# Kernel tuning notes

Hardware: AMD Instinct MI355X
Metric: run time of the kernel (lower is better)

## Reference

```python
import jax, jax.numpy as jnp
import numpy as np

N = 100000      # nodes
E = 640000      # edges
VOCAB = 100     # Embedding(num_embeddings=100)
EMB = 10        # embed_dim
H = 128         # GCN hidden width


def gcn_conv(x, W, b, src, dst, n):
    """PyG GCNConv: linear (no bias) -> add self loops -> sym-normalized scatter-add -> +bias."""
    x = x @ W                                  # [n, out]
    loop = jnp.arange(n, dtype=src.dtype)
    src2 = jnp.concatenate([src, loop])        # [E+n]
    dst2 = jnp.concatenate([dst, loop])
    deg = jax.ops.segment_sum(jnp.ones_like(dst2, dtype=x.dtype), dst2, num_segments=n)
    dinv = jnp.where(deg > 0, jax.lax.rsqrt(deg), 0.0)
    norm = dinv[src2] * dinv[dst2]             # [E+n]
    out = jax.ops.segment_sum(x[src2] * norm[:, None], dst2, num_segments=n)
    return out + b


def setup_inputs() -> dict:
    key = jax.random.key(0)
    ks = jax.random.split(key, 9)
    x = jax.random.randint(ks[0], (N, 1), 0, VOCAB, dtype=jnp.int32)
    edge_index = jax.random.randint(ks[1], (2, E), 0, N, dtype=jnp.int32)
    batch = jnp.zeros((N,), dtype=jnp.int32)
    emb = jax.random.normal(ks[2], (VOCAB, EMB), dtype=jnp.float32)
    W1 = jax.random.normal(ks[3], (EMB, H), dtype=jnp.float32) * 0.1
    b1 = jnp.zeros((H,), dtype=jnp.float32)
    W2 = jax.random.normal(ks[4], (H, H), dtype=jnp.float32) * 0.1
    b2 = jnp.zeros((H,), dtype=jnp.float32)
    W3 = jax.random.normal(ks[5], (H, 1), dtype=jnp.float32) * 0.1
    b3 = jnp.zeros((1,), dtype=jnp.float32)
    return {"x": x, "edge_index": edge_index, "batch": batch,
            "emb": emb, "W1": W1, "b1": b1, "W2": W2, "b2": b2, "W3": W3, "b3": b3}


def reference(x, edge_index, batch, emb, W1, b1, W2, b2, W3, b3):
    # eval mode: dropout(p=0.5) is identity
    h = emb[x[:, 0]]                           # [N, EMB] embedding lookup + squeeze
    src, dst = edge_index[0], edge_index[1]
    n = h.shape[0]
    h = jax.nn.relu(gcn_conv(h, W1, b1, src, dst, n))   # [N, 128]
    h = jax.nn.relu(gcn_conv(h, W2, b2, src, dst, n))   # [N, 128]
    out = jax.nn.sigmoid((h @ W3 + b3).reshape(-1))      # [N]
    return out
```

## Files before the change

### kernel.cpp

```cpp
#include <hip/hip_runtime.h>
#include <math.h>

#define HDIM 128
#define EMBD 10
#define CAP  32
#define ZSTRIDE 136

typedef __attribute__((ext_vector_type(8))) short short8;
typedef __attribute__((ext_vector_type(8))) unsigned short ushort8;
typedef __attribute__((ext_vector_type(4))) float float4a;
typedef __attribute__((ext_vector_type(2))) float float2a;
typedef __attribute__((ext_vector_type(2))) unsigned uint2a;
typedef __attribute__((ext_vector_type(4))) unsigned uint4a;

__device__ inline ushort bf16_rne(float f) {
    unsigned u = __float_as_uint(f);
    unsigned r = (u + 0x7fffu + ((u >> 16) & 1u)) >> 16;
    return (ushort)r;
}
__device__ inline float bf16_to_f(ushort u) {
    return __uint_as_float(((unsigned)u) << 16);
}

__global__ void k_prep(const float* __restrict__ emb, const float* __restrict__ W1,
                       const float* __restrict__ W2, ushort* __restrict__ Tb,
                       ushort* __restrict__ W2t, int* __restrict__ cnt,
                       int N, int vocab) {
    int t = blockIdx.x * 256 + threadIdx.x;
    if (t < N) cnt[t] = 0;
    if (t < vocab * HDIM) {
        int c = t >> 7, f = t & 127;
        float s = 0.f;
#pragma unroll
        for (int k = 0; k < EMBD; ++k) s += emb[c * EMBD + k] * W1[k * HDIM + f];
        Tb[t] = bf16_rne(s);
    }
    if (t < HDIM * HDIM) {
        int n = t >> 7, k = t & 127;
        W2t[t] = bf16_rne(W2[k * HDIM + n]);
    }
}

__global__ void k_fill(const int* __restrict__ src, const int* __restrict__ dst,
                       int* __restrict__ cnt, int* __restrict__ slot, int E) {
    int e = blockIdx.x * blockDim.x + threadIdx.x;
    if (e >= E) return;
    int d = dst[e];
    int p = atomicAdd(&cnt[d], 1);
    if (p < CAP) slot[(size_t)d * CAP + p] = src[e];
}

__global__ void k_meta(const int* __restrict__ x, const int* __restrict__ cnt,
                       unsigned* __restrict__ meta, int N) {
    int v = blockIdx.x * 256 + threadIdx.x;
    if (v >= N) return;
    meta[v] = ((unsigned)x[v] << 16) | (unsigned)bf16_rne(rsqrtf((float)cnt[v] + 1.0f));
}

__global__ __launch_bounds__(512) void k_gather1(const int* __restrict__ slot,
                                                 const int* __restrict__ cnt,
                                                 const unsigned* __restrict__ meta,
                                                 const ushort* __restrict__ Tb,
                                                 const float* __restrict__ b1,
                                                 unsigned char* __restrict__ Ap,
                                                 int N, int vocab) {
    __shared__ ushort TbL[100 * HDIM];
    int n8 = (vocab * HDIM) >> 3;
    for (int i = threadIdx.x; i < n8; i += 512)
        ((ushort8*)TbL)[i] = ((const ushort8*)Tb)[i];
    __syncthreads();

    int tid = blockIdx.x * 512 + threadIdx.x;
    int v = tid >> 4, q = tid & 15;
    if (v >= N) return;
    int deg = cnt[v];
    int m = min(deg, CAP);
    float dv = rsqrtf((float)deg + 1.0f);
    int total = m + 1;
    const int* slotv = slot + (size_t)v * CAP;

    float acc[8] = {0.f, 0.f, 0.f, 0.f, 0.f, 0.f, 0.f, 0.f};
    for (int base = 0; base < total; base += 8) {
        int4 sa = *(const int4*)(slotv + base);
        int4 sb = *(const int4*)(slotv + base + 4);
        int sv[8] = {sa.x, sa.y, sa.z, sa.w, sb.x, sb.y, sb.z, sb.w};
        const unsigned* mp[8];
#pragma unroll
        for (int t = 0; t < 8; ++t) {
            int idx = base + t;
            mp[t] = meta + ((idx < m) ? sv[t] : v);
        }
        unsigned m0, m1, m2, m3, m4, m5, m6, m7;
        asm volatile(
            "global_load_dword %0, %8, off\n\t"
            "global_load_dword %1, %9, off\n\t"
            "global_load_dword %2, %10, off\n\t"
            "global_load_dword %3, %11, off\n\t"
            "global_load_dword %4, %12, off\n\t"
            "global_load_dword %5, %13, off\n\t"
            "global_load_dword %6, %14, off\n\t"
            "global_load_dword %7, %15, off\n\t"
            "s_waitcnt vmcnt(0)"
            : "=&v"(m0), "=&v"(m1), "=&v"(m2), "=&v"(m3),
              "=&v"(m4), "=&v"(m5), "=&v"(m6), "=&v"(m7)
            : "v"(mp[0]), "v"(mp[1]), "v"(mp[2]), "v"(mp[3]),
              "v"(mp[4]), "v"(mp[5]), "v"(mp[6]), "v"(mp[7]));
        unsigned mm[8] = {m0, m1, m2, m3, m4, m5, m6, m7};
#pragma unroll
        for (int t = 0; t < 8; ++t) {
            float wt = (base + t <= m) ? bf16_to_f((ushort)(mm[t] & 0xffffu)) : 0.f;
            ushort8 y = *(const ushort8*)&TbL[(mm[t] >> 16) * HDIM + q * 8];
#pragma unroll
            for (int k = 0; k < 8; ++k) acc[k] += wt * bf16_to_f(y[k]);
        }
    }
    float4 bb0 = *(const float4*)(b1 + q * 8);
    float4 bb1 = *(const float4*)(b1 + q * 8 + 4);
    float bb[8] = {bb0.x, bb0.y, bb0.z, bb0.w, bb1.x, bb1.y, bb1.z, bb1.w};
    float o[8];
#pragma unroll
    for (int k = 0; k < 8; ++k)
        o[k] = dv * fmaxf(dv * acc[k] + bb[k], 0.f);
    unsigned lo = __builtin_amdgcn_cvt_pk_fp8_f32(o[0], o[1], 0u, false);
    lo = __builtin_amdgcn_cvt_pk_fp8_f32(o[2], o[3], lo, true);
    unsigned hi = __builtin_amdgcn_cvt_pk_fp8_f32(o[4], o[5], 0u, false);
    hi = __builtin_amdgcn_cvt_pk_fp8_f32(o[6], o[7], hi, true);
    uint2 ow = make_uint2(lo, hi);
    *(uint2*)(Ap + (size_t)v * HDIM + q * 8) = ow;
}

__global__ __launch_bounds__(256, 6) void k_conv2(const int* __restrict__ slot,
                                                  const int* __restrict__ cnt,
                                                  const unsigned char* __restrict__ Ap,
                                                  const ushort* __restrict__ W2t,
                                                  const float* __restrict__ b2,
                                                  const float* __restrict__ W3,
                                                  const float* __restrict__ b3,
                                                  float* __restrict__ out, int N) {
    __shared__ ushort Z[32 * ZSTRIDE];
    __shared__ float pbuf[4][16];
    int tid = threadIdx.x;
    int g = tid >> 3, q = tid & 7;
    int v0 = blockIdx.x * 32;
    int v = min(v0 + g, N - 1);

    int deg = cnt[v];
    int m = min(deg, CAP);
    float dv = rsqrtf((float)deg + 1.0f);
    int total = m + 1;
    const int* slotv = slot + (size_t)v * CAP;
    const unsigned char* aq = Ap + q * 16;

    float acc[16];
#pragma unroll
    for (int k = 0; k < 16; ++k) acc[k] = 0.f;

    for (int base = 0; base < total; base += 8) {
        int4 sa = *(const int4*)(slotv + base);
        int4 sb = *(const int4*)(slotv + base + 4);
        int sv[8] = {sa.x, sa.y, sa.z, sa.w, sb.x, sb.y, sb.z, sb.w};
        const unsigned char* pp[8];
#pragma unroll
        for (int t = 0; t < 8; ++t) {
            int idx = base + t;
            int s = (idx < m) ? sv[t] : v;
            pp[t] = aq + (size_t)s * HDIM;
        }
        uint4a r0, r1, r2, r3, r4, r5, r6, r7;
        asm volatile(
            "global_load_dwordx4 %0, %8, off\n\t"
            "global_load_dwordx4 %1, %9, off\n\t"
            "global_load_dwordx4 %2, %10, off\n\t"
            "global_load_dwordx4 %3, %11, off\n\t"
            "global_load_dwordx4 %4, %12, off\n\t"
            "global_load_dwordx4 %5, %13, off\n\t"
            "global_load_dwordx4 %6, %14, off\n\t"
            "global_load_dwordx4 %7, %15, off\n\t"
            "s_waitcnt vmcnt(0)"
            : "=&v"(r0), "=&v"(r1), "=&v"(r2), "=&v"(r3),
              "=&v"(r4), "=&v"(r5), "=&v"(r6), "=&v"(r7)
            : "v"(pp[0]), "v"(pp[1]), "v"(pp[2]), "v"(pp[3]),
              "v"(pp[4]), "v"(pp[5]), "v"(pp[6]), "v"(pp[7]));
        uint4a rr[8] = {r0, r1, r2, r3, r4, r5, r6, r7};
#pragma unroll
        for (int t = 0; t < 8; ++t) {
            float wt = (base + t <= m) ? 1.f : 0.f;
#pragma unroll
            for (int d = 0; d < 4; ++d) {
                float2a flo = __builtin_amdgcn_cvt_pk_f32_fp8(rr[t][d], false);
                float2a fhi = __builtin_amdgcn_cvt_pk_f32_fp8(rr[t][d], true);
                acc[d * 4 + 0] += wt * flo.x;
                acc[d * 4 + 1] += wt * flo.y;
                acc[d * 4 + 2] += wt * fhi.x;
                acc[d * 4 + 3] += wt * fhi.y;
            }
        }
    }
    ushort8 z0, z1;
#pragma unroll
    for (int k = 0; k < 8; ++k) {
        z0[k] = bf16_rne(dv * acc[k]);
        z1[k] = bf16_rne(dv * acc[8 + k]);
    }
    *(ushort8*)&Z[g * ZSTRIDE + q * 16] = z0;
    *(ushort8*)&Z[g * ZSTRIDE + q * 16 + 8] = z1;
    __syncthreads();

    int lane = tid & 63, w = tid >> 6;
    int l15 = lane & 15, g4 = lane >> 4;
    int rb = w >> 1, ch = w & 1;
    short8 af[4];
#pragma unroll
    for (int kt = 0; kt < 4; ++kt)
        af[kt] = *(const short8*)&Z[(rb * 16 + l15) * ZSTRIDE + kt * 32 + g4 * 8];

    float pr[4] = {0.f, 0.f, 0.f, 0.f};
#pragma unroll
    for (int i = 0; i < 4; ++i) {
        int nt = ch * 4 + i;
        int col = nt * 16 + l15;
        const ushort* bp = W2t + (size_t)col * HDIM + g4 * 8;
        float4a accD = {0.f, 0.f, 0.f, 0.f};
#pragma unroll
        for (int kt = 0; kt < 4; ++kt) {
            short8 bf = *(const short8*)(bp + kt * 32);
            accD = __builtin_amdgcn_mfma_f32_16x16x32_bf16(af[kt], bf, accD, 0, 0, 0);
        }
        float bc = b2[col], wc = W3[col];
#pragma unroll
        for (int r = 0; r < 4; ++r)
            pr[r] += fmaxf(accD[r] + bc, 0.f) * wc;
    }
#pragma unroll
    for (int off = 1; off < 16; off <<= 1) {
#pragma unroll
        for (int r = 0; r < 4; ++r) pr[r] += __shfl_xor(pr[r], off, 16);
    }
    if (l15 == 0) {
#pragma unroll
        for (int r = 0; r < 4; ++r) pbuf[w][g4 * 4 + r] = pr[r];
    }
    __syncthreads();
    if (tid < 32) {
        int row = tid;
        int rb2 = row >> 4, r15 = row & 15;
        float s = pbuf[2 * rb2][r15] + pbuf[2 * rb2 + 1][r15];
        int vr = v0 + row;
        if (vr < N) out[vr] = 1.f / (1.f + expf(-(s + b3[0])));
    }
}

extern "C" void kernel_launch(void* const* d_in, const int* in_sizes, int n_in,
                              void* d_out, int out_size, void* d_ws, size_t ws_size,
                              hipStream_t stream) {
    const int*   x    = (const int*)d_in[0];
    const int*   ei   = (const int*)d_in[1];
    const float* emb  = (const float*)d_in[3];
    const float* W1   = (const float*)d_in[4];
    const float* b1   = (const float*)d_in[5];
    const float* W2   = (const float*)d_in[6];
    const float* b2   = (const float*)d_in[7];
    const float* W3   = (const float*)d_in[8];
    const float* b3   = (const float*)d_in[9];
    float*       out  = (float*)d_out;

    int N = in_sizes[0];
    int E = in_sizes[1] / 2;
    int vocab = in_sizes[3] / EMBD;
    const int* src = ei;
    const int* dst = ei + E;

    char* w = (char*)d_ws;
    ushort*        Tb   = (ushort*)w;         w += (size_t)vocab * HDIM * 2;
    unsigned char* Ap   = (unsigned char*)w;  w += (size_t)N * HDIM;
    ushort*        W2t  = (ushort*)w;         w += (size_t)HDIM * HDIM * 2;
    int*           cnt  = (int*)w;            w += (size_t)N * 4;
    unsigned*      meta = (unsigned*)w;       w += (size_t)N * 4;
    int*           slot = (int*)w;            w += (size_t)N * CAP * 4 + 64;

    int prep_elems = N;
    if (vocab * HDIM > prep_elems) prep_elems = vocab * HDIM;
    if (HDIM * HDIM > prep_elems) prep_elems = HDIM * HDIM;
    k_prep<<<(prep_elems + 255) / 256, 256, 0, stream>>>(emb, W1, W2, Tb, W2t, cnt, N, vocab);
    k_fill<<<(E + 255) / 256, 256, 0, stream>>>(src, dst, cnt, slot, E);
    k_meta<<<(N + 255) / 256, 256, 0, stream>>>(x, cnt, meta, N);

    int g1blocks = (int)(((long long)N * 16 + 511) / 512);
    k_gather1<<<g1blocks, 512, 0, stream>>>(slot, cnt, meta, Tb, b1, Ap, N, vocab);

    int cblocks = (N + 31) / 32;
    k_conv2<<<cblocks, 256, 0, stream>>>(slot, cnt, Ap, W2t, b2, W3, b3, out, N);
}
```

Before: 174.8 us.

## Restructure gather1: 8 lanes per node, shuffle-shared meta, global table reads

The layer-1 gather now uses 8 threads per node, each producing 16 output features, so the grid is halved. Each lane loads one slot/meta entry and the 8 values are broadcast across the group with warp shuffles, replacing 8 redundant per-thread inline-asm gathers. The per-block copy of the embedding-projection table into LDS is removed, and rows are read directly from global memory, relying on L1/L2 caching of the small table. The change trades LDS setup and sync cost plus redundant meta loads for more registers per thread and table reads served from cache instead of LDS.

```diff
diff --git a/kernel.cpp b/kernel.cpp
--- a/kernel.cpp
+++ b/kernel.cpp
@@ -57,76 +57,81 @@
     meta[v] = ((unsigned)x[v] << 16) | (unsigned)bf16_rne(rsqrtf((float)cnt[v] + 1.0f));
 }
 
-__global__ __launch_bounds__(512) void k_gather1(const int* __restrict__ slot,
-                                                 const int* __restrict__ cnt,
-                                                 const unsigned* __restrict__ meta,
-                                                 const ushort* __restrict__ Tb,
-                                                 const float* __restrict__ b1,
-                                                 unsigned char* __restrict__ Ap,
-                                                 int N, int vocab) {
-    __shared__ ushort TbL[100 * HDIM];
-    int n8 = (vocab * HDIM) >> 3;
-    for (int i = threadIdx.x; i < n8; i += 512)
-        ((ushort8*)TbL)[i] = ((const ushort8*)Tb)[i];
-    __syncthreads();
-
+__global__ __launch_bounds__(512, 4) void k_gather1(const int* __restrict__ slot,
+                                                    const int* __restrict__ cnt,
+                                                    const unsigned* __restrict__ meta,
+                                                    const ushort* __restrict__ Tb,
+                                                    const float* __restrict__ b1,
+                                                    unsigned char* __restrict__ Ap,
+                                                    int N, int vocab) {
     int tid = blockIdx.x * 512 + threadIdx.x;
-    int v = tid >> 4, q = tid & 15;
+    int v = tid >> 3, q = tid & 7;
     if (v >= N) return;
+    int lane = threadIdx.x & 63;
+    int lbase = lane & 56;
     int deg = cnt[v];
     int m = min(deg, CAP);
     float dv = rsqrtf((float)deg + 1.0f);
     int total = m + 1;
     const int* slotv = slot + (size_t)v * CAP;
-
-    float acc[8] = {0.f, 0.f, 0.f, 0.f, 0.f, 0.f, 0.f, 0.f};
+    const ushort* tq = Tb + q * 16;
+
+    float acc[16];
+#pragma unroll
+    for (int k = 0; k < 16; ++k) acc[k] = 0.f;
+
     for (int base = 0; base < total; base += 8) {
-        int4 sa = *(const int4*)(slotv + base);
-        int4 sb = *(const int4*)(slotv + base + 4);
-        int sv[8] = {sa.x, sa.y, sa.z, sa.w, sb.x, sb.y, sb.z, sb.w};
-        const unsigned* mp[8];
-#pragma unroll
-        for (int t = 0; t < 8; ++t) {
-            int idx = base + t;
-            mp[t] = meta + ((idx < m) ? sv[t] : v);
-        }
-        unsigned m0, m1, m2, m3, m4, m5, m6, m7;
-        asm volatile(
-            "global_load_dword %0, %8, off\n\t"
-            "global_load_dword %1, %9, off\n\t"
-            "global_load_dword %2, %10, off\n\t"
-            "global_load_dword %3, %11, off\n\t"
-            "global_load_dword %4, %12, off\n\t"
-            "global_load_dword %5, %13, off\n\t"
-            "global_load_dword %6, %14, off\n\t"
-            "global_load_dword %7, %15, off\n\t"
-            "s_waitcnt vmcnt(0)"
-            : "=&v"(m0), "=&v"(m1), "=&v"(m2), "=&v"(m3),
-              "=&v"(m4), "=&v"(m5), "=&v"(m6), "=&v"(m7)
-            : "v"(mp[0]), "v"(mp[1]), "v"(mp[2]), "v"(mp[3]),
-              "v"(mp[4]), "v"(mp[5]), "v"(mp[6]), "v"(mp[7]));
-        unsigned mm[8] = {m0, m1, m2, m3, m4, m5, m6, m7};
-#pragma unroll
-        for (int t = 0; t < 8; ++t) {
-            float wt = (base + t <= m) ? bf16_to_f((ushort)(mm[t] & 0xffffu)) : 0.f;
-            ushort8 y = *(const ushort8*)&TbL[(mm[t] >> 16) * HDIM + q * 8];
-#pragma unroll
-            for (int k = 0; k < 8; ++k) acc[k] += wt * bf16_to_f(y[k]);
-        }
-    }
-    float4 bb0 = *(const float4*)(b1 + q * 8);
-    float4 bb1 = *(const float4*)(b1 + q * 8 + 4);
-    float bb[8] = {bb0.x, bb0.y, bb0.z, bb0.w, bb1.x, bb1.y, bb1.z, bb1.w};
-    float o[8];
-#pragma unroll
-    for (int k = 0; k < 8; ++k)
+        int idx = base + q;
+        int s = slotv[idx];
+        unsigned mv = meta[(idx < m) ? s : v];
+        unsigned mm[8];
+#pragma unroll
+        for (int t = 0; t < 8; ++t)
+            mm[t] = (unsigned)__shfl((int)mv, lbase + t, 64);
+
+#pragma unroll
+        for (int h = 0; h < 2; ++h) {
+            ushort8 ya[4], yb[4];
+#pragma unroll
+            for (int t = 0; t < 4; ++t) {
+                const ushort* rp = tq + (mm[h * 4 + t] >> 16) * HDIM;
+                ya[t] = *(const ushort8*)rp;
+                yb[t] = *(const ushort8*)(rp + 8);
+            }
+#pragma unroll
+            for (int t = 0; t < 4; ++t) {
+                int it = base + h * 4 + t;
+                float wt = (it <= m) ? bf16_to_f((ushort)(mm[h * 4 + t] & 0xffffu)) : 0.f;
+#pragma unroll
+                for (int k = 0; k < 8; ++k) {
+                    acc[k]     += wt * bf16_to_f((ushort)ya[t][k]);
+                    acc[8 + k] += wt * bf16_to_f((ushort)yb[t][k]);
+                }
+            }
+        }
+    }
+
+    float bb[16];
+#pragma unroll
+    for (int j = 0; j < 4; ++j) {
+        float4 b4 = *(const float4*)(b1 + q * 16 + j * 4);
+        bb[j * 4 + 0] = b4.x; bb[j * 4 + 1] = b4.y;
+        bb[j * 4 + 2] = b4.z; bb[j * 4 + 3] = b4.w;
+    }
+    float o[16];
+#pragma unroll
+    for (int k = 0; k < 16; ++k)
         o[k] = dv * fmaxf(dv * acc[k] + bb[k], 0.f);
-    unsigned lo = __builtin_amdgcn_cvt_pk_fp8_f32(o[0], o[1], 0u, false);
-    lo = __builtin_amdgcn_cvt_pk_fp8_f32(o[2], o[3], lo, true);
-    unsigned hi = __builtin_amdgcn_cvt_pk_fp8_f32(o[4], o[5], 0u, false);
-    hi = __builtin_amdgcn_cvt_pk_fp8_f32(o[6], o[7], hi, true);
-    uint2 ow = make_uint2(lo, hi);
-    *(uint2*)(Ap + (size_t)v * HDIM + q * 8) = ow;
+    unsigned d0 = __builtin_amdgcn_cvt_pk_fp8_f32(o[0], o[1], 0u, false);
+    d0 = __builtin_amdgcn_cvt_pk_fp8_f32(o[2], o[3], d0, true);
+    unsigned d1 = __builtin_amdgcn_cvt_pk_fp8_f32(o[4], o[5], 0u, false);
+    d1 = __builtin_amdgcn_cvt_pk_fp8_f32(o[6], o[7], d1, true);
+    unsigned d2 = __builtin_amdgcn_cvt_pk_fp8_f32(o[8], o[9], 0u, false);
+    d2 = __builtin_amdgcn_cvt_pk_fp8_f32(o[10], o[11], d2, true);
+    unsigned d3 = __builtin_amdgcn_cvt_pk_fp8_f32(o[12], o[13], 0u, false);
+    d3 = __builtin_amdgcn_cvt_pk_fp8_f32(o[14], o[15], d3, true);
+    uint4 ow = make_uint4(d0, d1, d2, d3);
+    *(uint4*)(Ap + (size_t)v * HDIM + q * 16) = ow;
 }
 
 __global__ __launch_bounds__(256, 6) void k_conv2(const int* __restrict__ slot,
@@ -285,7 +290,7 @@
     k_fill<<<(E + 255) / 256, 256, 0, stream>>>(src, dst, cnt, slot, E);
     k_meta<<<(N + 255) / 256, 256, 0, stream>>>(x, cnt, meta, N);
 
-    int g1blocks = (int)(((long long)N * 16 + 511) / 512);
+    int g1blocks = (int)(((long long)N * 8 + 511) / 512);
     k_gather1<<<g1blocks, 512, 0, stream>>>(slot, cnt, meta, Tb, b1, Ap, N, vocab);
 
     int cblocks = (N + 31) / 32;
```

After: 175.8 us (median of 2 runs). No clear change (+0.6%).
